# Kernel optimization log

Measured on AMD Instinct MI355X. Metric: run time of the kernel, lower is better.

## Reference

```python
import jax, jax.numpy as jnp
import numpy as np

BLOCK = 64      # BigBird block size
HEADS = 8
N_GLOBAL = 1
WINDOW = 1      # +/-1 block sliding window
N_RAND = 3


def _build_block_idx(n_blocks, seed=0):
    """Per query block: global + window + random key blocks, causal, deduped, -1 padded."""
    rng = np.random.RandomState(seed)
    m = N_GLOBAL + (2 * WINDOW + 1) + N_RAND  # 7
    idx = np.full((n_blocks, m), -1, np.int32)
    for i in range(n_blocks):
        s = set(range(min(N_GLOBAL, i + 1)))
        for w in range(i - WINDOW, i + 1):  # causal window (blocks <= i)
            if w >= 0:
                s.add(w)
        cand = [c for c in range(i + 1) if c not in s]
        rng.shuffle(cand)
        s.update(cand[:N_RAND])
        ss = sorted(s)
        idx[i, :len(ss)] = ss
    return idx


def setup_inputs() -> dict:
    key = jax.random.key(0)
    ks = jax.random.split(key, 12)
    b, S, D = 4, 4096, 768
    dff = 4 * D
    init = lambda k, shape: (0.02 * jax.random.normal(k, shape, jnp.float32))
    return {
        'q': jax.random.normal(ks[0], (b, S, D), jnp.float32),
        'ln1_g': jnp.ones((D,), jnp.float32), 'ln1_b': jnp.zeros((D,), jnp.float32),
        'Wq': init(ks[1], (D, D)), 'bq': jnp.zeros((D,), jnp.float32),
        'Wk': init(ks[2], (D, D)), 'bk': jnp.zeros((D,), jnp.float32),
        'Wv': init(ks[3], (D, D)), 'bv': jnp.zeros((D,), jnp.float32),
        'Wo': init(ks[4], (D, D)), 'bo': jnp.zeros((D,), jnp.float32),
        'ln2_g': jnp.ones((D,), jnp.float32), 'ln2_b': jnp.zeros((D,), jnp.float32),
        'W1': init(ks[5], (D, dff)), 'b1': jnp.zeros((dff,), jnp.float32),
        'W2': init(ks[6], (dff, D)), 'b2': jnp.zeros((D,), jnp.float32),
        'key_block_idx': jnp.asarray(_build_block_idx(S // BLOCK), jnp.int32),
    }


def _layernorm(x, g, b, eps=1e-5):
    mu = jnp.mean(x, axis=-1, keepdims=True)
    var = jnp.mean(jnp.square(x - mu), axis=-1, keepdims=True)
    return (x - mu) * jax.lax.rsqrt(var + eps) * g + b


def _bigbird_attn(x, Wq, bq, Wk, bk, Wv, bv, Wo, bo, key_block_idx):
    b, S, D = x.shape
    H, hd = HEADS, D // HEADS
    nb = S // BLOCK
    m = key_block_idx.shape[1]
    proj = lambda W, bias: (x @ W + bias).reshape(b, nb, BLOCK, H, hd).transpose(0, 3, 1, 2, 4)
    q = proj(Wq, bq)  # [b,h,nb,B,hd]
    k = proj(Wk, bk)
    v = proj(Wv, bv)
    valid = key_block_idx >= 0                      # [nb, m]
    idx = jnp.maximum(key_block_idx, 0)
    kg = k[:, :, idx]                               # [b,h,nb,m,B,hd]
    vg = v[:, :, idx]
    scores = jnp.einsum('bhnqd,bhnmkd->bhnqmk', q, kg) / jnp.sqrt(jnp.float32(hd))
    off = jnp.arange(BLOCK)
    qpos = jnp.arange(nb)[:, None] * BLOCK + off    # [nb, B]
    kpos = idx[..., None] * BLOCK + off             # [nb, m, B]
    mask = valid[:, :, None] & (kpos[:, None, :, :] <= qpos[:, :, None, None])  # [nb,q,m,k]
    scores = jnp.where(mask[None, None], scores, jnp.float32(-1e9))
    attn = jax.nn.softmax(scores.reshape(b, H, nb, BLOCK, m * BLOCK), axis=-1)
    attn = attn.reshape(b, H, nb, BLOCK, m, BLOCK)
    out = jnp.einsum('bhnqmk,bhnmkd->bhnqd', attn, vg)   # [b,h,nb,B,hd]
    out = out.transpose(0, 2, 3, 1, 4).reshape(b, S, D)
    return out @ Wo + bo


def reference(q, ln1_g, ln1_b, Wq, bq, Wk, bk, Wv, bv, Wo, bo,
              ln2_g, ln2_b, W1, b1, W2, b2, key_block_idx):
    # pre-norm residual: x + attn(ln1(x))
    x = q + _bigbird_attn(_layernorm(q, ln1_g, ln1_b), Wq, bq, Wk, bk, Wv, bv, Wo, bo, key_block_idx)
    h = _layernorm(x, ln2_g, ln2_b)
    x = x + (jax.nn.gelu(h @ W1 + b1) @ W2 + b2)
    return x
```

## Files before the change

kernel.cpp:

```cpp
#include <hip/hip_runtime.h>
#include <cstdint>

typedef __bf16  bf16x8 __attribute__((ext_vector_type(8)));
typedef float   f32x4  __attribute__((ext_vector_type(4)));

__device__ __forceinline__ float bf2f(uint16_t u) {
    uint32_t x = ((uint32_t)u) << 16;
    float f; __builtin_memcpy(&f, &x, 4); return f;
}
__device__ __forceinline__ uint16_t f2bf(float f) {
    uint32_t x; __builtin_memcpy(&x, &f, 4);
    uint32_t r = (x + 0x7fffu + ((x >> 16) & 1u)) >> 16;
    return (uint16_t)r;
}
__device__ __forceinline__ float gelu_f(float x) {
    float y = 0.7978845608028654f * (x + 0.044715f * x * x * x);
    float e = __expf(-2.0f * y);
    return x * __builtin_amdgcn_rcpf(1.0f + e);
}
__device__ __forceinline__ float ldf(const void* p, size_t i, int f) {
    return f ? ((const float*)p)[i] : bf2f(((const uint16_t*)p)[i]);
}

__device__ __forceinline__ void gl_lds16(const void* g, void* lds) {
    __builtin_amdgcn_global_load_lds(
        (const __attribute__((address_space(1))) void*)g,
        (__attribute__((address_space(3))) void*)lds,
        16, 0, 0);
}

#define BATCH 4
#define SEQ   4096
#define DMODEL 768
#define HEADS 8
#define HDIM  96
#define DFF   3072
#define NBLK  64
#define MKEYS 7
#define MROWS 16384

#define SWZ(b) ((b) ^ ((((b) >> 8) & 7) << 4))

__global__ void sniff_k(const uint32_t* __restrict__ g, int* __restrict__ flag) {
    if (threadIdx.x == 0) flag[0] = (g[0] == 0x3F800000u) ? 1 : 0;
}

__global__ void transpose_k(const void* __restrict__ in, uint16_t* __restrict__ out,
                            int R, int C, const int* __restrict__ flag) {
    __shared__ float t[32][33];
    const int f = flag[0];
    int bx = blockIdx.x * 32, by = blockIdx.y * 32;
    int tx = threadIdx.x, ty = threadIdx.y;
    #pragma unroll
    for (int i = 0; i < 32; i += 8)
        t[ty + i][tx] = ldf(in, (size_t)(by + ty + i) * C + bx + tx, f);
    __syncthreads();
    #pragma unroll
    for (int i = 0; i < 32; i += 8)
        out[(size_t)(bx + ty + i) * R + by + tx] = f2bf(t[tx][ty + i]);
}

__global__ void concat_bias_k(const void* bq, const void* bk, const void* bv,
                              uint16_t* out, const int* __restrict__ flag) {
    const int f = flag[0];
    int i = blockIdx.x * 256 + threadIdx.x;
    if (i < DMODEL) {
        out[i]              = f2bf(ldf(bq, i, f));
        out[DMODEL + i]     = f2bf(ldf(bk, i, f));
        out[2 * DMODEL + i] = f2bf(ldf(bv, i, f));
    }
}

__global__ __launch_bounds__(256) void ln_k(const void* __restrict__ x,
                                            const void* __restrict__ g,
                                            const void* __restrict__ b,
                                            uint16_t* __restrict__ y,
                                            int xmode, const int* __restrict__ flag) {
    const int f = flag[0];
    const int xf = xmode ? f : 0;
    int row = blockIdx.x, tid = threadIdx.x;
    size_t base = (size_t)row * DMODEL;
    float v0 = ldf(x, base + tid, xf);
    float v1 = ldf(x, base + tid + 256, xf);
    float v2 = ldf(x, base + tid + 512, xf);
    float s = v0 + v1 + v2;
    float s2 = v0 * v0 + v1 * v1 + v2 * v2;
    #pragma unroll
    for (int off = 1; off < 64; off <<= 1) {
        s  += __shfl_xor(s, off, 64);
        s2 += __shfl_xor(s2, off, 64);
    }
    __shared__ float rs[4], rs2[4];
    if ((tid & 63) == 0) { rs[tid >> 6] = s; rs2[tid >> 6] = s2; }
    __syncthreads();
    s = rs[0] + rs[1] + rs[2] + rs[3];
    s2 = rs2[0] + rs2[1] + rs2[2] + rs2[3];
    float mu = s * (1.0f / DMODEL);
    float var = s2 * (1.0f / DMODEL) - mu * mu;
    float rstd = rsqrtf(var + 1e-5f);
    uint16_t* yr = y + base;
    yr[tid]       = f2bf((v0 - mu) * rstd * ldf(g, tid, f)       + ldf(b, tid, f));
    yr[tid + 256] = f2bf((v1 - mu) * rstd * ldf(g, tid + 256, f) + ldf(b, tid + 256, f));
    yr[tid + 512] = f2bf((v2 - mu) * rstd * ldf(g, tid + 512, f) + ldf(b, tid + 512, f));
}

template <int EPI>
__global__ __launch_bounds__(512, 2) void gemm256(
        const uint16_t* __restrict__ A, const uint16_t* __restrict__ Bt,
        const void* __restrict__ bias, const void* __restrict__ resid,
        void* __restrict__ C, int M, int N, int K,
        int bmode, int rmode, int omode, const int* __restrict__ flag) {
    __shared__ __align__(16) uint16_t SMEM[65536];
    const int f = flag[0];
    const int bf = bmode ? f : 0, rf = rmode ? f : 0, of = omode ? f : 0;
    const int tid = threadIdx.x;
    const int lane = tid & 63, wave = tid >> 6;
    const int l15 = lane & 15, quad = lane >> 4;
    const int wr = wave >> 2, wc = wave & 3;

    const int GX = gridDim.x;
    const int flat = blockIdx.y * GX + blockIdx.x;
    const int xcd = flat & 7, w8 = flat >> 3;
    const int cb = w8 % GX;
    const int rb = (w8 / GX) * 8 + xcd;
    const int m0 = rb * 256, n0 = cb * 256;
    const int NT = K >> 6;

    const uint32_t swz = ((uint32_t)((l15 >> 1) & 7)) << 4;
    const uint32_t tk0 = ((uint32_t)(quad * 16)) ^ swz;
    const uint32_t tk1 = ((uint32_t)(64 + quad * 16)) ^ swz;
    const uint32_t aA0 = (uint32_t)((wr * 64 + l15) * 128) + tk0;
    const uint32_t aA1 = (uint32_t)((wr * 64 + l15) * 128) + tk1;
    const uint32_t aB0 = 65536u + (uint32_t)((wc * 32 + l15) * 128) + tk0;
    const uint32_t aB1 = 65536u + (uint32_t)((wc * 32 + l15) * 128) + tk1;
    const char* const smb = (const char*)SMEM;

    uint32_t goff0, goff1;
    {
        uint32_t pb0 = (uint32_t)tid * 16u;
        uint32_t e0  = SWZ(pb0) >> 1;
        goff0 = (e0 >> 6) * (uint32_t)K + (e0 & 63u);
        uint32_t pb1 = (uint32_t)(512 + tid) * 16u;
        uint32_t e1  = SWZ(pb1) >> 1;
        goff1 = (e1 >> 6) * (uint32_t)K + (e1 & 63u);
    }

    f32x4 acc[2][4][2][2] = {};
    bf16x8 af[4][2], bfr[2][2][2];

    auto stage = [&](const uint16_t* __restrict__ P, int row0, int kt, uint16_t* slot) {
        const uint16_t* gb = P + (size_t)row0 * (size_t)K + (size_t)kt * 64u;
        gl_lds16(gb + goff0, slot + wave * 512);
        gl_lds16(gb + goff1, slot + 4096 + wave * 512);
    };

#define SA_(db,h)  (SMEM + ((db)*2+(h))*8192)
#define SB_(db,h)  (SMEM + 32768 + ((db)*2+(h))*8192)
#define LDA(DB,MIH) { _Pragma("unroll") for (int mi = 0; mi < 4; ++mi) {           \
      af[mi][0] = *(const bf16x8*)(smb + ((((DB)*2+(MIH))*16384) + mi*2048) + aA0);\
      af[mi][1] = *(const bf16x8*)(smb + ((((DB)*2+(MIH))*16384) + mi*2048) + aA1);} }
#define LDB(DB) { _Pragma("unroll") for (int h = 0; h < 2; ++h)                    \
      _Pragma("unroll") for (int nj = 0; nj < 2; ++nj) {                           \
      bfr[h][nj][0] = *(const bf16x8*)(smb + ((((DB)*2+h)*16384) + nj*2048) + aB0);\
      bfr[h][nj][1] = *(const bf16x8*)(smb + ((((DB)*2+h)*16384) + nj*2048) + aB1);} }
#define MM(MIH) { _Pragma("unroll") for (int ks = 0; ks < 2; ++ks)                 \
      _Pragma("unroll") for (int mi = 0; mi < 4; ++mi)                             \
      _Pragma("unroll") for (int h = 0; h < 2; ++h)                                \
      _Pragma("unroll") for (int nj = 0; nj < 2; ++nj)                             \
        acc[MIH][mi][h][nj] = __builtin_amdgcn_mfma_f32_16x16x32_bf16(             \
            af[mi][ks], bfr[h][nj][ks], acc[MIH][mi][h][nj], 0, 0, 0); }
#define BAR1  asm volatile("s_barrier" ::: "memory");                              \
              asm volatile("s_waitcnt lgkmcnt(0)" ::: "memory");                   \
              __builtin_amdgcn_sched_barrier(0)
#define PRIO1 __builtin_amdgcn_s_setprio(1)
#define PRIO0 __builtin_amdgcn_s_setprio(0); __builtin_amdgcn_sched_barrier(0)
#define BAR2  asm volatile("s_barrier" ::: "memory")

    stage(A,  m0,       0, SA_(0,0));
    stage(A,  m0 + 128, 0, SA_(0,1));
    stage(Bt, n0,       0, SB_(0,0));
    stage(Bt, n0 + 128, 0, SB_(0,1));
    stage(A,  m0,       1, SA_(1,0));
    stage(Bt, n0,       1, SB_(1,0));
    stage(Bt, n0 + 128, 1, SB_(1,1));
    asm volatile("s_waitcnt vmcnt(6)" ::: "memory");
    BAR2;

    #pragma unroll 1
    for (int tt = 0; tt < NT; tt += 2) {
        const bool last = (tt + 2 >= NT);
        LDA(0, 0); LDB(0);
        stage(A, m0 + 128, tt + 1, SA_(1,1));
        BAR1; PRIO1; MM(0); PRIO0;
        BAR2;
        LDA(0, 1);
        if (!last) { stage(A,  m0,       tt + 2, SA_(0,0));
                     stage(Bt, n0,       tt + 2, SB_(0,0));
                     stage(Bt, n0 + 128, tt + 2, SB_(0,1)); }
        BAR1; PRIO1; MM(1); PRIO0;
        if (last) { asm volatile("s_waitcnt vmcnt(2)" ::: "memory"); }
        else      { asm volatile("s_waitcnt vmcnt(8)" ::: "memory"); }
        BAR2;
        LDA(1, 0); LDB(1);
        if (!last) stage(A, m0 + 128, tt + 2, SA_(0,1));
        BAR1; PRIO1; MM(0); PRIO0;
        if (last) { asm volatile("s_waitcnt vmcnt(0)" ::: "memory"); }
        else      { asm volatile("s_waitcnt vmcnt(8)" ::: "memory"); }
        BAR2;
        LDA(1, 1);
        if (!last) { stage(A,  m0,       tt + 3, SA_(1,0));
                     stage(Bt, n0,       tt + 3, SB_(1,0));
                     stage(Bt, n0 + 128, tt + 3, SB_(1,1)); }
        BAR1; PRIO1; MM(1); PRIO0;
        if (!last) { asm volatile("s_waitcnt vmcnt(6)" ::: "memory"); }
        BAR2;
    }
#undef SA_
#undef SB_
#undef LDA
#undef LDB
#undef MM
#undef BAR1
#undef PRIO1
#undef PRIO0
#undef BAR2

    float bv[2][2];
    #pragma unroll
    for (int njh = 0; njh < 2; ++njh)
        #pragma unroll
        for (int nj = 0; nj < 2; ++nj)
            bv[njh][nj] = ldf(bias, n0 + njh * 128 + wc * 32 + nj * 16 + l15, bf);

    #pragma unroll
    for (int mih = 0; mih < 2; ++mih)
    #pragma unroll
    for (int mi = 0; mi < 4; ++mi) {
        int rowb = m0 + mih * 128 + wr * 64 + mi * 16 + quad * 4;
        #pragma unroll
        for (int njh = 0; njh < 2; ++njh)
        #pragma unroll
        for (int nj = 0; nj < 2; ++nj) {
            int col = n0 + njh * 128 + wc * 32 + nj * 16 + l15;
            #pragma unroll
            for (int r = 0; r < 4; ++r) {
                float v = acc[mih][mi][njh][nj][r] + bv[njh][nj];
                if (EPI == 2) v = gelu_f(v);
                size_t off = (size_t)(rowb + r) * N + col;
                if (EPI == 1) v += ldf(resid, off, rf);
                if (of) ((float*)C)[off] = v;
                else    ((uint16_t*)C)[off] = f2bf(v);
            }
        }
    }
}

__global__ __launch_bounds__(256, 4) void attn_k(const __bf16* __restrict__ QKV,
                                                 const int* __restrict__ kbi,
                                                 uint16_t* __restrict__ Aout) {
    const int qb = blockIdx.x;
    const int h  = blockIdx.y;
    const int bb = blockIdx.z;
    const int tid = threadIdx.x;
    const int lane = tid & 63, wave = tid >> 6;
    const int l15 = lane & 15, quad = lane >> 4;
    const int h8 = l15 >> 3;

    __shared__ __align__(16) __bf16 Ks[64 * 96];
    __shared__ __align__(16) __bf16 VTs[96 * 72];
    __shared__ __align__(16) __bf16 Ps[4 * 16 * 72];

    char* const ksb = (char*)Ks;
    char* const vtb = (char*)VTs;
    char* const psb = (char*)Ps + wave * 2304;

    const int tq = bb * SEQ + qb * 64;
    const int r0row = wave * 16 + quad * 4;
    const float sc = 0.10206207262f;

    int nv[4];
    #pragma unroll
    for (int r = 0; r < 4; ++r) {
        int cnt = 0;
        #pragma unroll
        for (int m = 0; m < MKEYS; ++m)
            cnt += (kbi[(r0row + r) * MKEYS + m] >= 0) ? 1 : 0;
        nv[r] = cnt;
    }

    bf16x8 aq[3];
    {
        const __bf16* qp = QKV + (size_t)(tq + wave * 16 + l15) * 2304 + h * HDIM + quad * 8;
        aq[0] = *(const bf16x8*)(qp);
        aq[1] = *(const bf16x8*)(qp + 32);
        aq[2] = *(const bf16x8*)(qp + 64);
    }

    uint32_t goff[3], kwb[3], vtw[3];
    #pragma unroll
    for (int i = 0; i < 3; ++i) {
        int c = i * 256 + tid;
        int r = c / 12, cm = c % 12;
        goff[i] = (uint32_t)(r * 2304 + cm * 8);
        kwb[i]  = (uint32_t)(r * 192 + ((cm ^ (r & 3)) << 4));
        vtw[i]  = (uint32_t)(cm * 8 * 144 + ((r * 2) ^ ((cm & 7) << 4)));
    }

    bf16x8 kreg[3], vreg[3];
    auto load_tile = [&](int kb) {
        const __bf16* base = QKV + (size_t)(bb * SEQ + kb * 64) * 2304 + h * HDIM;
        #pragma unroll
        for (int i = 0; i < 3; ++i) {
            kreg[i] = *(const bf16x8*)(base + DMODEL + goff[i]);
            vreg[i] = *(const bf16x8*)(base + 2 * DMODEL + goff[i]);
        }
    };
    auto write_tile = [&]() {
        #pragma unroll
        for (int i = 0; i < 3; ++i) {
            *(bf16x8*)(ksb + kwb[i]) = kreg[i];
            #pragma unroll
            for (int j2 = 0; j2 < 8; ++j2)
                *(__bf16*)(vtb + vtw[i] + j2 * 144) = vreg[i][j2];
        }
    };

    int kb0 = kbi[qb * MKEYS + 0];
    int kb_cur = kb0 < 0 ? 0 : kb0;
    load_tile(kb_cur);
    write_tile();
    __syncthreads();

    float mrun[4] = {-1e30f, -1e30f, -1e30f, -1e30f};
    float lrun[4] = {0.f, 0.f, 0.f, 0.f};
    f32x4 oacc[6] = {};

    const uint32_t kq16 = (uint32_t)((quad ^ (l15 & 3)) << 4);
    const uint32_t prB  = (uint32_t)((quad << 4) ^ ((l15 >> 2) << 4));
    const uint32_t vq   = (uint32_t)(((quad ^ h8) << 4));

    for (int mi = 0; mi < MKEYS; ++mi) {
        int kb_nxt = 0;
        if (mi + 1 < MKEYS) {
            kb_nxt = kbi[qb * MKEYS + mi + 1];
            kb_nxt = kb_nxt < 0 ? 0 : kb_nxt;
            load_tile(kb_nxt);
        }

        f32x4 s[4] = {};
        __builtin_amdgcn_s_setprio(1);
        #pragma unroll
        for (int kt = 0; kt < 3; ++kt) {
            #pragma unroll
            for (int j = 0; j < 4; ++j) {
                bf16x8 bk = *(const bf16x8*)(ksb + (j * 16 + l15) * 192 + kt * 64 + kq16);
                s[j] = __builtin_amdgcn_mfma_f32_16x16x32_bf16(aq[kt], bk, s[j], 0, 0, 0);
            }
        }
        __builtin_amdgcn_s_setprio(0);

        const bool diag = (kb_cur == qb);
        #pragma unroll
        for (int r = 0; r < 4; ++r) {
            const bool rowen = (mi < nv[r]);
            float mx = -1e30f;
            #pragma unroll
            for (int j = 0; j < 4; ++j) {
                float v = s[j][r] * sc;
                if (!rowen || (diag && (j * 16 + l15 > r0row + r))) v = -1e30f;
                s[j][r] = v;
                mx = fmaxf(mx, v);
            }
            #pragma unroll
            for (int off = 1; off < 16; off <<= 1) mx = fmaxf(mx, __shfl_xor(mx, off, 64));
            float mnew = fmaxf(mrun[r], mx);
            float alpha = __expf(mrun[r] - mnew);
            mrun[r] = mnew;
            float ls = 0.f;
            #pragma unroll
            for (int j = 0; j < 4; ++j) {
                float p = __expf(s[j][r] - mnew);
                s[j][r] = p;
                ls += p;
            }
            #pragma unroll
            for (int off = 1; off < 16; off <<= 1) ls += __shfl_xor(ls, off, 64);
            lrun[r] = lrun[r] * alpha + ls;
            #pragma unroll
            for (int t = 0; t < 6; ++t) oacc[t][r] *= alpha;
            #pragma unroll
            for (int j = 0; j < 4; ++j)
                *(__bf16*)(psb + (quad * 4 + r) * 144 +
                           (((uint32_t)(j * 32) | (uint32_t)(l15 * 2)) ^ ((uint32_t)quad << 4)))
                    = (__bf16)s[j][r];
        }

        asm volatile("s_waitcnt lgkmcnt(0)" ::: "memory");
        __builtin_amdgcn_sched_barrier(0);

        __builtin_amdgcn_s_setprio(1);
        #pragma unroll
        for (int kt = 0; kt < 2; ++kt) {
            bf16x8 ap = *(const bf16x8*)(psb + l15 * 144 + kt * 64 + prB);
            #pragma unroll
            for (int t = 0; t < 6; ++t) {
                const uint32_t L = (uint32_t)((((2 * t) & 7) << 4) ^ (kt << 6));
                bf16x8 bv = *(const bf16x8*)(vtb + (t * 16 + l15) * 144 +
                                             ((uint32_t)(quad << 4) ^ (uint32_t)(h8 << 4) ^ L));
                oacc[t] = __builtin_amdgcn_mfma_f32_16x16x32_bf16(ap, bv, oacc[t], 0, 0, 0);
            }
        }
        __builtin_amdgcn_s_setprio(0);

        if (mi + 1 < MKEYS) {
            __syncthreads();
            write_tile();
            __syncthreads();
            kb_cur = kb_nxt;
        }
    }

    #pragma unroll
    for (int r = 0; r < 4; ++r) {
        float inv = 1.0f / lrun[r];
        int token = tq + r0row + r;
        #pragma unroll
        for (int t = 0; t < 6; ++t) {
            int col = h * HDIM + t * 16 + l15;
            Aout[(size_t)token * DMODEL + col] = f2bf(oacc[t][r] * inv);
        }
    }
}

extern "C" void kernel_launch(void* const* d_in, const int* in_sizes, int n_in,
                              void* d_out, int out_size, void* d_ws, size_t ws_size,
                              hipStream_t stream) {
    const void* q     = d_in[0];
    const void* ln1_g = d_in[1];
    const void* ln1_b = d_in[2];
    const void* Wq    = d_in[3];
    const void* bq    = d_in[4];
    const void* Wk    = d_in[5];
    const void* bk    = d_in[6];
    const void* Wv    = d_in[7];
    const void* bv    = d_in[8];
    const void* Wo    = d_in[9];
    const void* bo    = d_in[10];
    const void* ln2_g = d_in[11];
    const void* ln2_b = d_in[12];
    const void* W1    = d_in[13];
    const void* b1    = d_in[14];
    const void* W2    = d_in[15];
    const void* b2    = d_in[16];
    const int*  kbi   = (const int*)d_in[17];
    char* ws = (char*)d_ws;

    uint16_t* WqkvT = (uint16_t*)(ws + 0);
    uint16_t* WoT   = (uint16_t*)(ws + 3538944);
    uint16_t* W1T   = (uint16_t*)(ws + 4718592);
    uint16_t* W2T   = (uint16_t*)(ws + 9437184);
    uint16_t* bqkv  = (uint16_t*)(ws + 14155776);
    int*      flag  = (int*)(ws + 14160384);
    uint16_t* x1    = (uint16_t*)(ws + 14160896);
    uint16_t* QKV   = (uint16_t*)(ws + 39326720);
    uint16_t* attn  = (uint16_t*)(ws + 114824192);
    uint16_t* xb    = (uint16_t*)(ws + 139990016);
    uint16_t* mid   = QKV;

    sniff_k<<<1, 64, 0, stream>>>((const uint32_t*)ln1_g, flag);

    dim3 tb(32, 8);
    transpose_k<<<dim3(24, 24), tb, 0, stream>>>(Wq, WqkvT, DMODEL, DMODEL, flag);
    transpose_k<<<dim3(24, 24), tb, 0, stream>>>(Wk, WqkvT + DMODEL * DMODEL, DMODEL, DMODEL, flag);
    transpose_k<<<dim3(24, 24), tb, 0, stream>>>(Wv, WqkvT + 2 * DMODEL * DMODEL, DMODEL, DMODEL, flag);
    transpose_k<<<dim3(24, 24), tb, 0, stream>>>(Wo, WoT, DMODEL, DMODEL, flag);
    transpose_k<<<dim3(96, 24), tb, 0, stream>>>(W1, W1T, DMODEL, DFF, flag);
    transpose_k<<<dim3(24, 96), tb, 0, stream>>>(W2, W2T, DFF, DMODEL, flag);
    concat_bias_k<<<3, 256, 0, stream>>>(bq, bk, bv, bqkv, flag);

    ln_k<<<MROWS, 256, 0, stream>>>(q, ln1_g, ln1_b, x1, 1, flag);
    gemm256<0><<<dim3(9, 64), 512, 0, stream>>>(x1, WqkvT, bqkv, nullptr, QKV,
                                                MROWS, 3 * DMODEL, DMODEL, 0, 0, 0, flag);
    attn_k<<<dim3(NBLK, HEADS, BATCH), 256, 0, stream>>>((const __bf16*)QKV, kbi, attn);
    gemm256<1><<<dim3(3, 64), 512, 0, stream>>>(attn, WoT, bo, q, xb,
                                                MROWS, DMODEL, DMODEL, 1, 1, 0, flag);
    ln_k<<<MROWS, 256, 0, stream>>>(xb, ln2_g, ln2_b, x1, 0, flag);
    gemm256<2><<<dim3(12, 64), 512, 0, stream>>>(x1, W1T, b1, nullptr, mid,
                                                 MROWS, DFF, DMODEL, 1, 0, 0, flag);
    gemm256<1><<<dim3(3, 64), 512, 0, stream>>>(mid, W2T, b2, xb, d_out,
                                                MROWS, DMODEL, DFF, 1, 0, 1, flag);
}
```

Measured before the change: 634.2 us.

## Replace 256x256 GEMM with 128x256 tile, K=32 triple-buffered pipeline

Rewrites the projection and MLP GEMM kernel to use 128x256 output tiles with 32-wide K steps, a three-stage LDS ring buffer, and a new XOR swizzle, in place of the 256x256 tile with 64-wide K steps and double buffering. The grid doubles along M, and launch bounds ask for 4 blocks per CU instead of 2, using about 72KB of LDS. The aim is more blocks in flight and better latency hiding. In exchange, each loaded byte is reused less, global and LDS traffic per FLOP rises, and there are more barriers per K step. The loop unrolls by 3 over NT; with K=768 and K=3072, NT is divisible by 3.

```diff
diff --git a/kernel.cpp b/kernel.cpp
--- a/kernel.cpp
+++ b/kernel.cpp
@@ -38,8 +38,6 @@
 #define NBLK  64
 #define MKEYS 7
 #define MROWS 16384
-
-#define SWZ(b) ((b) ^ ((((b) >> 8) & 7) << 4))
 
 __global__ void sniff_k(const uint32_t* __restrict__ g, int* __restrict__ flag) {
     if (threadIdx.x == 0) flag[0] = (g[0] == 0x3F800000u) ? 1 : 0;
@@ -105,14 +103,14 @@
 }
 
 template <int EPI>
-__global__ __launch_bounds__(512, 2) void gemm256(
+__global__ __launch_bounds__(512, 4) void gemm128(
         const uint16_t* __restrict__ A, const uint16_t* __restrict__ Bt,
         const void* __restrict__ bias, const void* __restrict__ resid,
         void* __restrict__ C, int M, int N, int K,
         int bmode, int rmode, int omode, const int* __restrict__ flag) {
-    __shared__ __align__(16) uint16_t SMEM[65536];
+    __shared__ __align__(16) uint16_t SMEM[36864];
     const int f = flag[0];
-    const int bf = bmode ? f : 0, rf = rmode ? f : 0, of = omode ? f : 0;
+    const int bf_ = bmode ? f : 0, rf = rmode ? f : 0, of = omode ? f : 0;
     const int tid = threadIdx.x;
     const int lane = tid & 63, wave = tid >> 6;
     const int l15 = lane & 15, quad = lane >> 4;
@@ -123,128 +121,82 @@
     const int xcd = flat & 7, w8 = flat >> 3;
     const int cb = w8 % GX;
     const int rb = (w8 / GX) * 8 + xcd;
-    const int m0 = rb * 256, n0 = cb * 256;
-    const int NT = K >> 6;
-
-    const uint32_t swz = ((uint32_t)((l15 >> 1) & 7)) << 4;
-    const uint32_t tk0 = ((uint32_t)(quad * 16)) ^ swz;
-    const uint32_t tk1 = ((uint32_t)(64 + quad * 16)) ^ swz;
-    const uint32_t aA0 = (uint32_t)((wr * 64 + l15) * 128) + tk0;
-    const uint32_t aA1 = (uint32_t)((wr * 64 + l15) * 128) + tk1;
-    const uint32_t aB0 = 65536u + (uint32_t)((wc * 32 + l15) * 128) + tk0;
-    const uint32_t aB1 = 65536u + (uint32_t)((wc * 32 + l15) * 128) + tk1;
+    const int m0 = rb * 128, n0 = cb * 256;
+    const int NT = K >> 5;
+
+    const uint32_t cxor = ((uint32_t)(quad ^ ((l15 >> 2) & 3))) << 4;
+    const uint32_t aA = (uint32_t)((wr * 64 + l15) * 64) + cxor;
+    const uint32_t aB = 24576u + (uint32_t)((wc * 64 + l15) * 64) + cxor;
     const char* const smb = (const char*)SMEM;
 
-    uint32_t goff0, goff1;
-    {
-        uint32_t pb0 = (uint32_t)tid * 16u;
-        uint32_t e0  = SWZ(pb0) >> 1;
-        goff0 = (e0 >> 6) * (uint32_t)K + (e0 & 63u);
-        uint32_t pb1 = (uint32_t)(512 + tid) * 16u;
-        uint32_t e1  = SWZ(pb1) >> 1;
-        goff1 = (e1 >> 6) * (uint32_t)K + (e1 & 63u);
-    }
-
-    f32x4 acc[2][4][2][2] = {};
-    bf16x8 af[4][2], bfr[2][2][2];
-
-    auto stage = [&](const uint16_t* __restrict__ P, int row0, int kt, uint16_t* slot) {
-        const uint16_t* gb = P + (size_t)row0 * (size_t)K + (size_t)kt * 64u;
-        gl_lds16(gb + goff0, slot + wave * 512);
-        gl_lds16(gb + goff1, slot + 4096 + wave * 512);
+    const uint32_t goffA = (uint32_t)((tid >> 2) * K + (((tid & 3) ^ ((tid >> 4) & 3)) << 3));
+
+    f32x4 acc[4][4] = {};
+    bf16x8 af[4], bfr[4];
+
+    const uint16_t* const Abase = A + (size_t)m0 * K;
+    const uint16_t* const Bbase = Bt + (size_t)n0 * K;
+
+    auto stage = [&](int t, int s) {
+        const uint16_t* ga = Abase + t * 32 + goffA;
+        const uint16_t* gb = Bbase + t * 32 + goffA;
+        uint16_t* da = SMEM + s * 4096 + wave * 512;
+        uint16_t* db = SMEM + 12288 + s * 8192 + wave * 512;
+        gl_lds16(ga, da);
+        gl_lds16(gb, db);
+        gl_lds16(gb + (size_t)128 * K, db + 4096);
     };
 
-#define SA_(db,h)  (SMEM + ((db)*2+(h))*8192)
-#define SB_(db,h)  (SMEM + 32768 + ((db)*2+(h))*8192)
-#define LDA(DB,MIH) { _Pragma("unroll") for (int mi = 0; mi < 4; ++mi) {           \
-      af[mi][0] = *(const bf16x8*)(smb + ((((DB)*2+(MIH))*16384) + mi*2048) + aA0);\
-      af[mi][1] = *(const bf16x8*)(smb + ((((DB)*2+(MIH))*16384) + mi*2048) + aA1);} }
-#define LDB(DB) { _Pragma("unroll") for (int h = 0; h < 2; ++h)                    \
-      _Pragma("unroll") for (int nj = 0; nj < 2; ++nj) {                           \
-      bfr[h][nj][0] = *(const bf16x8*)(smb + ((((DB)*2+h)*16384) + nj*2048) + aB0);\
-      bfr[h][nj][1] = *(const bf16x8*)(smb + ((((DB)*2+h)*16384) + nj*2048) + aB1);} }
-#define MM(MIH) { _Pragma("unroll") for (int ks = 0; ks < 2; ++ks)                 \
-      _Pragma("unroll") for (int mi = 0; mi < 4; ++mi)                             \
-      _Pragma("unroll") for (int h = 0; h < 2; ++h)                                \
-      _Pragma("unroll") for (int nj = 0; nj < 2; ++nj)                             \
-        acc[MIH][mi][h][nj] = __builtin_amdgcn_mfma_f32_16x16x32_bf16(             \
-            af[mi][ks], bfr[h][nj][ks], acc[MIH][mi][h][nj], 0, 0, 0); }
-#define BAR1  asm volatile("s_barrier" ::: "memory");                              \
-              asm volatile("s_waitcnt lgkmcnt(0)" ::: "memory");                   \
-              __builtin_amdgcn_sched_barrier(0)
-#define PRIO1 __builtin_amdgcn_s_setprio(1)
-#define PRIO0 __builtin_amdgcn_s_setprio(0); __builtin_amdgcn_sched_barrier(0)
-#define BAR2  asm volatile("s_barrier" ::: "memory")
-
-    stage(A,  m0,       0, SA_(0,0));
-    stage(A,  m0 + 128, 0, SA_(0,1));
-    stage(Bt, n0,       0, SB_(0,0));
-    stage(Bt, n0 + 128, 0, SB_(0,1));
-    stage(A,  m0,       1, SA_(1,0));
-    stage(Bt, n0,       1, SB_(1,0));
-    stage(Bt, n0 + 128, 1, SB_(1,1));
-    asm volatile("s_waitcnt vmcnt(6)" ::: "memory");
-    BAR2;
+#define LD(S) { _Pragma("unroll") for (int mi = 0; mi < 4; ++mi)                     \
+        af[mi] = *(const bf16x8*)(smb + (S) * 8192 + mi * 1024 + aA);                \
+      _Pragma("unroll") for (int nj = 0; nj < 4; ++nj)                               \
+        bfr[nj] = *(const bf16x8*)(smb + (S) * 16384 + nj * 1024 + aB); }
+#define MM { _Pragma("unroll") for (int mi = 0; mi < 4; ++mi)                        \
+      _Pragma("unroll") for (int nj = 0; nj < 4; ++nj)                               \
+        acc[mi][nj] = __builtin_amdgcn_mfma_f32_16x16x32_bf16(                       \
+            af[mi], bfr[nj], acc[mi][nj], 0, 0, 0); }
+#define PH(S, T) {                                                                   \
+    if ((T) + 2 < NT) stage((T) + 2, ((S) + 2) % 3);                                 \
+    LD(S);                                                                           \
+    asm volatile("s_waitcnt lgkmcnt(0)" ::: "memory");                               \
+    __builtin_amdgcn_sched_barrier(0);                                               \
+    __builtin_amdgcn_s_setprio(1);                                                   \
+    MM;                                                                              \
+    __builtin_amdgcn_s_setprio(0);                                                   \
+    __builtin_amdgcn_sched_barrier(0);                                               \
+    if ((T) + 2 < NT)      { asm volatile("s_waitcnt vmcnt(3)" ::: "memory"); }      \
+    else if ((T) + 1 < NT) { asm volatile("s_waitcnt vmcnt(0)" ::: "memory"); }      \
+    asm volatile("s_barrier" ::: "memory"); }
+
+    stage(0, 0);
+    stage(1, 1);
+    asm volatile("s_waitcnt vmcnt(3)" ::: "memory");
+    asm volatile("s_barrier" ::: "memory");
 
     #pragma unroll 1
-    for (int tt = 0; tt < NT; tt += 2) {
-        const bool last = (tt + 2 >= NT);
-        LDA(0, 0); LDB(0);
-        stage(A, m0 + 128, tt + 1, SA_(1,1));
-        BAR1; PRIO1; MM(0); PRIO0;
-        BAR2;
-        LDA(0, 1);
-        if (!last) { stage(A,  m0,       tt + 2, SA_(0,0));
-                     stage(Bt, n0,       tt + 2, SB_(0,0));
-                     stage(Bt, n0 + 128, tt + 2, SB_(0,1)); }
-        BAR1; PRIO1; MM(1); PRIO0;
-        if (last) { asm volatile("s_waitcnt vmcnt(2)" ::: "memory"); }
-        else      { asm volatile("s_waitcnt vmcnt(8)" ::: "memory"); }
-        BAR2;
-        LDA(1, 0); LDB(1);
-        if (!last) stage(A, m0 + 128, tt + 2, SA_(0,1));
-        BAR1; PRIO1; MM(0); PRIO0;
-        if (last) { asm volatile("s_waitcnt vmcnt(0)" ::: "memory"); }
-        else      { asm volatile("s_waitcnt vmcnt(8)" ::: "memory"); }
-        BAR2;
-        LDA(1, 1);
-        if (!last) { stage(A,  m0,       tt + 3, SA_(1,0));
-                     stage(Bt, n0,       tt + 3, SB_(1,0));
-                     stage(Bt, n0 + 128, tt + 3, SB_(1,1)); }
-        BAR1; PRIO1; MM(1); PRIO0;
-        if (!last) { asm volatile("s_waitcnt vmcnt(6)" ::: "memory"); }
-        BAR2;
-    }
-#undef SA_
-#undef SB_
-#undef LDA
-#undef LDB
+    for (int t = 0; t < NT; t += 3) {
+        PH(0, t)
+        PH(1, t + 1)
+        PH(2, t + 2)
+    }
+#undef LD
 #undef MM
-#undef BAR1
-#undef PRIO1
-#undef PRIO0
-#undef BAR2
-
-    float bv[2][2];
-    #pragma unroll
-    for (int njh = 0; njh < 2; ++njh)
-        #pragma unroll
-        for (int nj = 0; nj < 2; ++nj)
-            bv[njh][nj] = ldf(bias, n0 + njh * 128 + wc * 32 + nj * 16 + l15, bf);
-
-    #pragma unroll
-    for (int mih = 0; mih < 2; ++mih)
+#undef PH
+
+    float bv[4];
+    #pragma unroll
+    for (int nj = 0; nj < 4; ++nj)
+        bv[nj] = ldf(bias, n0 + wc * 64 + nj * 16 + l15, bf_);
+
     #pragma unroll
     for (int mi = 0; mi < 4; ++mi) {
-        int rowb = m0 + mih * 128 + wr * 64 + mi * 16 + quad * 4;
-        #pragma unroll
-        for (int njh = 0; njh < 2; ++njh)
-        #pragma unroll
-        for (int nj = 0; nj < 2; ++nj) {
-            int col = n0 + njh * 128 + wc * 32 + nj * 16 + l15;
+        int rowb = m0 + wr * 64 + mi * 16 + quad * 4;
+        #pragma unroll
+        for (int nj = 0; nj < 4; ++nj) {
+            int col = n0 + wc * 64 + nj * 16 + l15;
             #pragma unroll
             for (int r = 0; r < 4; ++r) {
-                float v = acc[mih][mi][njh][nj][r] + bv[njh][nj];
+                float v = acc[mi][nj][r] + bv[nj];
                 if (EPI == 2) v = gelu_f(v);
                 size_t off = (size_t)(rowb + r) * N + col;
                 if (EPI == 1) v += ldf(resid, off, rf);
@@ -337,7 +289,6 @@
 
     const uint32_t kq16 = (uint32_t)((quad ^ (l15 & 3)) << 4);
     const uint32_t prB  = (uint32_t)((quad << 4) ^ ((l15 >> 2) << 4));
-    const uint32_t vq   = (uint32_t)(((quad ^ h8) << 4));
 
     for (int mi = 0; mi < MKEYS; ++mi) {
         int kb_nxt = 0;
@@ -479,14 +430,14 @@
     concat_bias_k<<<3, 256, 0, stream>>>(bq, bk, bv, bqkv, flag);
 
     ln_k<<<MROWS, 256, 0, stream>>>(q, ln1_g, ln1_b, x1, 1, flag);
-    gemm256<0><<<dim3(9, 64), 512, 0, stream>>>(x1, WqkvT, bqkv, nullptr, QKV,
-                                                MROWS, 3 * DMODEL, DMODEL, 0, 0, 0, flag);
+    gemm128<0><<<dim3(9, 128), 512, 0, stream>>>(x1, WqkvT, bqkv, nullptr, QKV,
+                                                 MROWS, 3 * DMODEL, DMODEL, 0, 0, 0, flag);
     attn_k<<<dim3(NBLK, HEADS, BATCH), 256, 0, stream>>>((const __bf16*)QKV, kbi, attn);
-    gemm256<1><<<dim3(3, 64), 512, 0, stream>>>(attn, WoT, bo, q, xb,
-                                                MROWS, DMODEL, DMODEL, 1, 1, 0, flag);
+    gemm128<1><<<dim3(3, 128), 512, 0, stream>>>(attn, WoT, bo, q, xb,
+                                                 MROWS, DMODEL, DMODEL, 1, 1, 0, flag);
     ln_k<<<MROWS, 256, 0, stream>>>(xb, ln2_g, ln2_b, x1, 0, flag);
-    gemm256<2><<<dim3(12, 64), 512, 0, stream>>>(x1, W1T, b1, nullptr, mid,
-                                                 MROWS, DFF, DMODEL, 1, 0, 0, flag);
-    gemm256<1><<<dim3(3, 64), 512, 0, stream>>>(mid, W2T, b2, xb, d_out,
-                                                MROWS, DMODEL, DFF, 1, 0, 1, flag);
-}
+    gemm128<2><<<dim3(12, 128), 512, 0, stream>>>(x1, W1T, b1, nullptr, mid,
+                                                  MROWS, DFF, DMODEL, 1, 0, 0, flag);
+    gemm128<1><<<dim3(3, 128), 512, 0, stream>>>(mid, W2T, b2, xb, d_out,
+                                                 MROWS, DMODEL, DFF, 1, 0, 1, flag);
+}
```

Result: faster. 586.3 us (-7.5%).
